# Performance work log

Hardware: AMD Instinct MI355X
Metric: run time of the kernel (lower is better)

Reference implementation:

```python
import jax, jax.numpy as jnp
import numpy as np
import itertools

VOXEL_SIZE = np.array([0.05, 0.05, 0.1], np.float32)   # xyz, from cfg.voxel_size
GRID_OFFSET = np.array([0.0, -40.0, -3.0], np.float32)  # xyz, cfg.grid_bounds[:3]
BN_EPS = 1e-3

# ---------------- rulebook construction (numpy, mirrors spconv indice pairs) ----------------

def _enc(c, shape):
    Z, Y, X = shape
    c = c.astype(np.int64)
    return ((c[:, 0] * Z + c[:, 1]) * Y + c[:, 2]) * X + c[:, 3]

def _lookup(sk, order, q):
    pos = np.clip(np.searchsorted(sk, q), 0, len(sk) - 1)
    return np.where((q >= 0) & (sk[pos] == q), order[pos], -1).astype(np.int32)

def _subm_rulebook(coords, shape):
    # submanifold conv k=3, pad=1: output sites == input sites; neighbor = out + (k-1)
    keys = _enc(coords, shape)
    order = np.argsort(keys).astype(np.int32)
    sk = keys[order]
    dims = np.array(shape)
    rows = []
    for off in itertools.product((-1, 0, 1), repeat=3):
        nb = coords[:, 1:] + np.array(off)
        inb = ((nb >= 0) & (nb < dims)).all(1)
        full = np.concatenate([coords[:, :1], nb], 1)
        q = np.where(inb, _enc(full, shape), -1)
        rows.append(_lookup(sk, order, q))
    return np.stack(rows)  # [27, N] input index or -1

def _strided_rulebook(coords, shape_in, ksize, stride, pad):
    # regular sparse conv: out active = any site receiving a contribution; in = out*s - p + k
    ksize = np.array(ksize); stride = np.array(stride); pad = np.array(pad)
    shape_out = tuple((((np.array(shape_in) + 2 * pad - ksize) // stride) + 1).tolist())
    keys = _enc(coords, shape_in)
    order = np.argsort(keys).astype(np.int32)
    sk = keys[order]
    cand = []
    for k in itertools.product(*[range(int(x)) for x in ksize]):
        num = coords[:, 1:] + pad - np.array(k)
        ok = (num % stride == 0).all(1)
        o = num // stride
        ok &= (o >= 0).all(1) & (o < np.array(shape_out)).all(1)
        cand.append(np.concatenate([coords[ok, :1], o[ok]], 1))
    out_coords = np.unique(np.concatenate(cand, 0), axis=0).astype(np.int32)
    dims_in = np.array(shape_in)
    rows = []
    for k in itertools.product(*[range(int(x)) for x in ksize]):
        ic = out_coords[:, 1:] * stride - pad + np.array(k)
        inb = ((ic >= 0) & (ic < dims_in)).all(1)
        full = np.concatenate([out_coords[:, :1], ic], 1)
        q = np.where(inb, _enc(full, shape_in), -1)
        rows.append(_lookup(sk, order, q))
    return out_coords, np.stack(rows), shape_out

# ---------------- inputs ----------------

def setup_inputs() -> dict:
    rng = np.random.default_rng(0)
    B, NPB = 2, 8000
    shape0 = (41, 1600, 1280)
    parts = []
    for b in range(B):
        c = np.stack([rng.integers(0, shape0[0], 4 * NPB),
                      rng.integers(0, shape0[1], 4 * NPB),
                      rng.integers(0, shape0[2], 4 * NPB)], 1)
        c = np.unique(c, axis=0)[:NPB]
        parts.append(np.concatenate([np.full((len(c), 1), b), c], 1))
    coords0 = np.concatenate(parts, 0).astype(np.int32)

    rb0 = _subm_rulebook(coords0, shape0)
    coords1, rbc1, shape1 = _strided_rulebook(coords0, shape0, (3, 3, 3), (2, 2, 2), (1, 1, 1))
    rb1 = _subm_rulebook(coords1, shape1)
    coords2, rbc2, shape2 = _strided_rulebook(coords1, shape1, (3, 3, 3), (2, 2, 2), (1, 1, 1))
    rb2 = _subm_rulebook(coords2, shape2)
    coords3, rbc3, shape3 = _strided_rulebook(coords2, shape2, (3, 3, 3), (2, 2, 2), (0, 1, 1))
    rb3 = _subm_rulebook(coords3, shape3)
    coords4, rbc4, shape4 = _strided_rulebook(coords3, shape3, (3, 1, 1), (2, 1, 1), (0, 0, 0))

    def w(*s):
        return jnp.asarray((rng.standard_normal(s) * 0.1).astype(np.float32))

    inp = {"features": jnp.asarray(rng.standard_normal((len(coords0), 4)).astype(np.float32))}
    specs = [("1a", 27, 4, 16), ("1b", 27, 16, 16), ("1c", 27, 16, 32),
             ("2a", 27, 32, 32), ("2b", 27, 32, 32), ("2c", 27, 32, 64),
             ("3a", 27, 64, 64), ("3b", 27, 64, 64), ("3c", 27, 64, 64), ("3d", 27, 64, 64),
             ("4a", 27, 64, 64), ("4b", 27, 64, 64), ("4c", 27, 64, 64), ("4d", 3, 64, 64)]
    for name, K, ci, co in specs:
        inp["w" + name] = w(K, ci, co)
        inp["g" + name] = jnp.asarray((np.abs(rng.standard_normal(co)) + 0.5).astype(np.float32))
        inp["b" + name] = jnp.asarray((rng.standard_normal(co) * 0.1).astype(np.float32))
    inp.update(coordinates=jnp.asarray(coords0), coords1=jnp.asarray(coords1),
               coords2=jnp.asarray(coords2), coords3=jnp.asarray(coords3),
               rb0=jnp.asarray(rb0), rbc1=jnp.asarray(rbc1), rb1=jnp.asarray(rb1),
               rbc2=jnp.asarray(rbc2), rb2=jnp.asarray(rb2), rbc3=jnp.asarray(rbc3),
               rb3=jnp.asarray(rb3), rbc4=jnp.asarray(rbc4), batch_size=B)
    return inp

# ---------------- forward math ----------------

def _sconv(feat, rb, W):
    # gather-GEMM-scatter: rb[k,n] = input row feeding output n via kernel offset k (-1 = none)
    out = jnp.zeros((rb.shape[1], W.shape[2]), feat.dtype)
    for k in range(W.shape[0]):
        idx = rb[k]
        g = jnp.where(idx[:, None] >= 0, feat[jnp.clip(idx, 0)], 0.0)
        out = out + g @ W[k]
    return out

def _bn_relu(x, g, b):
    # BatchNorm1d in training mode over active voxels (biased var), eps=1e-3, then ReLU
    m = jnp.mean(x, 0)
    v = jnp.mean(jnp.square(x - m), 0)
    return jax.nn.relu((x - m) * (g / jnp.sqrt(v + BN_EPS)) + b)

def reference(features, w1a, g1a, b1a, w1b, g1b, b1b, w1c, g1c, b1c,
              w2a, g2a, b2a, w2b, g2b, b2b, w2c, g2c, b2c,
              w3a, g3a, b3a, w3b, g3b, b3b, w3c, g3c, b3c, w3d, g3d, b3d,
              w4a, g4a, b4a, w4b, g4b, b4b, w4c, g4c, b4c, w4d, g4d, b4d,
              coordinates, coords1, coords2, coords3,
              rb0, rbc1, rb1, rbc2, rb2, rbc3, rb3, rbc4, batch_size):
    f0 = features
    h = _bn_relu(_sconv(f0, rb0, w1a), g1a, b1a)
    h = _bn_relu(_sconv(h, rb0, w1b), g1b, b1b)
    f1 = _bn_relu(_sconv(h, rbc1, w1c), g1c, b1c)
    h = _bn_relu(_sconv(f1, rb1, w2a), g2a, b2a)
    h = _bn_relu(_sconv(h, rb1, w2b), g2b, b2b)
    f2 = _bn_relu(_sconv(h, rbc2, w2c), g2c, b2c)
    h = _bn_relu(_sconv(f2, rb2, w3a), g3a, b3a)
    h = _bn_relu(_sconv(h, rb2, w3b), g3b, b3b)
    h = _bn_relu(_sconv(h, rb2, w3c), g3c, b3c)
    f3 = _bn_relu(_sconv(h, rbc3, w3d), g3d, b3d)
    h = _bn_relu(_sconv(f3, rb3, w4a), g4a, b4a)
    h = _bn_relu(_sconv(h, rb3, w4b), g4b, b4b)
    h = _bn_relu(_sconv(h, rb3, w4c), g4c, b4c)
    f4 = _bn_relu(_sconv(h, rbc4, w4d), g4d, b4d)

    vs = jnp.asarray(VOXEL_SIZE)
    off = jnp.asarray(GRID_OFFSET)
    def to_global(stride, c):
        # indices are (b,z,y,x); flip -> (x,y,z,b); take xyz
        return jnp.flip(c, 1)[:, :3].astype(jnp.float32) * (vs * stride) + off
    xyz0 = to_global(1, coordinates)
    xyz1 = to_global(2, coords1)
    xyz2 = to_global(4, coords2)
    xyz3 = to_global(8, coords3)
    return (xyz0, f0, xyz1, f1, xyz2, f2, xyz3, f3, f4)
```

## Files before the change

### kernel.cpp

```cpp
#include <hip/hip_runtime.h>

#define BN_EPS 1e-3f
#define NREP 16

typedef __attribute__((ext_vector_type(8))) short short8;
typedef __attribute__((ext_vector_type(4))) float float4v;

__device__ __forceinline__ short f2bf(float f) {
    unsigned u = __float_as_uint(f);
    unsigned r = (u + 0x7FFFu + ((u >> 16) & 1u)) >> 16;
    return (short)r;
}

template <int N>
__device__ __forceinline__ void waitcnt_vm() {
    __builtin_amdgcn_s_waitcnt(0xF70 | (N & 15) | ((N >> 4) << 14));
}

__device__ __forceinline__ void wave_barrier() { asm volatile("s_barrier" ::: "memory"); }

__device__ __forceinline__ void dma16(const short* g, short* l) {
    __builtin_amdgcn_global_load_lds((const __attribute__((address_space(1))) void*)g,
                                     (__attribute__((address_space(3))) void*)l, 16, 0, 0);
}


__global__ __launch_bounds__(256) void zero_kernel(float* p, int n) {
    int i = blockIdx.x * 256 + threadIdx.x;
    if (i < n) p[i] = 0.f;
}

__global__ __launch_bounds__(256) void copy_kernel(const float* __restrict__ in,
                                                   float* __restrict__ out, int n) {
    int i = blockIdx.x * 256 + threadIdx.x;
    if (i < n) out[i] = in[i];
}

__global__ __launch_bounds__(256) void zero_rows_kernel(short* a, short* b, long maxN) {
    int t = threadIdx.x;
    if (t < 32) a[maxN * 32 + t] = 0;
    else if (t < 96) a[maxN * 64 + (t - 32)] = 0;
    else if (t < 128) b[maxN * 32 + (t - 96)] = 0;
    else if (t < 192) b[maxN * 64 + (t - 128)] = 0;
}

__global__ __launch_bounds__(256) void xyz_kernel(const int* __restrict__ coords,
                                                  float* __restrict__ out, int N,
                                                  float sx, float sy, float sz) {
    int n = blockIdx.x * 256 + threadIdx.x;
    if (n >= N) return;
    int4 c = ((const int4*)coords)[n];
    out[n * 3 + 0] = c.w * sx;
    out[n * 3 + 1] = c.z * sy - 40.0f;
    out[n * 3 + 2] = c.y * sz - 3.0f;
}

__global__ __launch_bounds__(256) void convert_f0(const float* __restrict__ f,
                                                  short* __restrict__ dst, int N) {
    int i = blockIdx.x * 256 + threadIdx.x;
    if (i >= N * 32) return;
    int c = i & 31, n = i >> 5;
    dst[i] = (c < 4) ? f2bf(f[n * 4 + c]) : (short)0;
}

struct PrepAll {
    const float* src[14];
    short* dst[14];
    int CI[14];
    int CO[14];
    int CHP[14];
    int cum[15];
};

__global__ __launch_bounds__(256) void prep_all_kernel(PrepAll d) {
    int i = blockIdx.x * 256 + threadIdx.x;
    if (i >= d.cum[14]) return;
    int l = 0;
    while (l < 13 && i >= d.cum[l + 1]) ++l;
    int f = i - d.cum[l];
    int CO = d.CO[l], CI = d.CI[l];
    int NCH = d.CHP[l] / 32, CT = CO / 16;
    int e = f & 7;
    int u = f >> 3;
    int l16 = u & 15;
    int q = (u >> 4) & 3;
    int u2 = u >> 6;
    int t = u2 % CT;
    int c = (u2 / CT) % NCH;
    int k = u2 / (CT * NCH);
    int ci = c * 32 + q * 8 + e;
    int co = t * 16 + l16;
    float v = (ci < CI) ? d.src[l][((size_t)k * CI + ci) * CO + co] : 0.f;
    d.dst[l][f] = f2bf(v);
}

struct ASet {
    short8 v0, v1, v2, v3;
};

template <int CHP, int CO, int K>
__global__ __launch_bounds__(256, 4) void sconv_hyb(const short* __restrict__ feat,
                                                    const int* __restrict__ rb,
                                                    const short* __restrict__ Wt,
                                                    float* __restrict__ out,
                                                    float* __restrict__ stats, int N, int zrow) {
    constexpr int NCH = CHP / 32;
    constexpr int CT = CO / 16;
    constexpr int BTILE = CO * CHP;
    constexpr int NB = BTILE / 512;
    constexpr int A = 2 * NCH;
    constexpr int ROWS = 128;

    __shared__ __align__(16) short ldsB[3 * BTILE];
    __shared__ int sIdx[K * ROWS];
    __shared__ int sFlag[K];
    __shared__ int sKl[K];
    __shared__ int sKn;

    const int tid = threadIdx.x;
    const int w = tid >> 6;
    const int lane = tid & 63;
    const int quad = lane >> 4;
    const int l16 = lane & 15;
    const int m0 = blockIdx.x * ROWS;

    if (tid < K) sFlag[tid] = 0;
    __syncthreads();
    for (int e = tid; e < K * ROWS; e += 256) {
        int r = m0 + (e & (ROWS - 1));
        int v = (r < N) ? rb[(size_t)(e >> 7) * N + r] : -1;
        sIdx[e] = v;
        if (v >= 0) sFlag[e >> 7] = 1;
    }
    __syncthreads();
    if (w == 0) {
        int f = (lane < K) ? sFlag[lane] : 0;
        unsigned long long m = __ballot(f != 0);
        if (f) sKl[__popcll(m & ((1ull << lane) - 1ull))] = lane;
        if (lane == 0) sKn = (int)__popcll(m);
    }
    __syncthreads();
    const int nk = sKn;

    const short* fquad = feat + quad * 8;

    auto issueB = [&](int kp, int slot) {
        const short* wk = Wt + (size_t)kp * BTILE + lane * 8;
        short* bb = ldsB + slot * BTILE;
#pragma unroll
        for (int jj = 0; jj < (NB + 3) / 4; ++jj) {
            int j = jj * 4 + w;
            if (j < NB) dma16(wk + j * 512, bb + j * 512);
        }
    };
    auto issueA = [&](int kp) {
        ASet s;
        int i0 = sIdx[kp * ROWS + w * 32 + l16];
        int i1 = sIdx[kp * ROWS + w * 32 + 16 + l16];
        const short* p0 = fquad + (size_t)(i0 < 0 ? zrow : i0) * CHP;
        const short* p1 = fquad + (size_t)(i1 < 0 ? zrow : i1) * CHP;
        s.v0 = *(const short8*)p0;
        s.v2 = *(const short8*)p1;
        if constexpr (NCH == 2) {
            s.v1 = *(const short8*)(p0 + 32);
            s.v3 = *(const short8*)(p1 + 32);
        } else {
            s.v1 = (short8)0;
            s.v3 = (short8)0;
        }
        return s;
    };

    float4v acc[2][CT];
#pragma unroll
    for (int mt = 0; mt < 2; ++mt)
#pragma unroll
        for (int t = 0; t < CT; ++t) acc[mt][t] = (float4v)0.f;

    constexpr int BW0 = NB / 4 + ((NB % 4) > 0 ? 1 : 0);
    constexpr int BW1 = NB / 4 + ((NB % 4) > 1 ? 1 : 0);
    constexpr int BW2 = NB / 4 + ((NB % 4) > 2 ? 1 : 0);
    constexpr int BW3 = NB / 4;

    ASet sA{}, sB{}, sC{};
    if (nk > 0) {
        issueB(sKl[0], 0);
        sA = issueA(sKl[0]);
    }
    if (nk > 1) {
        issueB(sKl[1], 1);
        sB = issueA(sKl[1]);
    }

    int slotRd = 0, slotWr = 2;
    for (int i = 0; i < nk; ++i) {
        if (i < nk - 1) {
            if (w == 0) waitcnt_vm<BW0 + A>();
            else if (w == 1) waitcnt_vm<BW1 + A>();
            else if (w == 2) waitcnt_vm<BW2 + A>();
            else waitcnt_vm<BW3 + A>();
        } else {
            waitcnt_vm<0>();
        }
        __builtin_amdgcn_sched_barrier(0);
        wave_barrier();
        if (i + 2 < nk) {
            issueB(sKl[i + 2], slotWr);
            sC = issueA(sKl[i + 2]);
        }
        const short* bb = ldsB + slotRd * BTILE;
#pragma unroll
        for (int c = 0; c < NCH; ++c) {
#pragma unroll
            for (int t = 0; t < CT; ++t) {
                short8 bf = *(const short8*)(bb + ((c * CT + t) * 64 + quad * 16 + l16) * 8);
#pragma unroll
                for (int mt = 0; mt < 2; ++mt) {
                    short8 af = (mt == 0) ? ((c == 0) ? sA.v0 : sA.v1)
                                          : ((c == 0) ? sA.v2 : sA.v3);
                    acc[mt][t] = __builtin_amdgcn_mfma_f32_16x16x32_bf16(af, bf, acc[mt][t], 0,
                                                                         0, 0);
                }
            }
        }
        sA = sB;
        sB = sC;
        slotRd = (slotRd == 2) ? 0 : slotRd + 1;
        slotWr = (slotWr == 2) ? 0 : slotWr + 1;
    }

#pragma unroll
    for (int mt = 0; mt < 2; ++mt)
#pragma unroll
        for (int t = 0; t < CT; ++t) {
            int col = t * 16 + l16;
#pragma unroll
            for (int r = 0; r < 4; ++r) {
                int orow = m0 + w * 32 + mt * 16 + quad * 4 + r;
                if (orow < N) out[(size_t)orow * CO + col] = acc[mt][t][r];
            }
        }

    __syncthreads();
    float* red = (float*)ldsB;
#pragma unroll
    for (int t = 0; t < CT; ++t) {
        float s = 0.f, ss = 0.f;
#pragma unroll
        for (int mt = 0; mt < 2; ++mt)
#pragma unroll
            for (int r = 0; r < 4; ++r) {
                float v = acc[mt][t][r];
                s += v;
                ss += v * v;
            }
        s += __shfl_xor(s, 16);
        s += __shfl_xor(s, 32);
        ss += __shfl_xor(ss, 16);
        ss += __shfl_xor(ss, 32);
        if (lane < 16) {
            red[w * 2 * CO + t * 16 + lane] = s;
            red[w * 2 * CO + CO + t * 16 + lane] = ss;
        }
    }
    __syncthreads();
    if (tid < 2 * CO) {
        float v = red[tid] + red[2 * CO + tid] + red[4 * CO + tid] + red[6 * CO + tid];
        float* st = stats + (size_t)(blockIdx.x & (NREP - 1)) * 128;
        atomicAdd(&st[(tid < CO) ? tid : (64 + tid - CO)], v);
    }
}

template <int COUT, int CHPN, bool F32OUT, bool BFOUT>
__global__ __launch_bounds__(256) void bn_apply(const float* __restrict__ x,
                                                const float* __restrict__ stats,
                                                const float* __restrict__ g,
                                                const float* __restrict__ b,
                                                float* __restrict__ fout,
                                                short* __restrict__ bfout, int N) {
    constexpr int CW = BFOUT ? CHPN : COUT;
    __shared__ float ssc[COUT];
    __shared__ float ssh[COUT];
    int tid = threadIdx.x;
    if (tid < COUT) {
        float s = 0.f, q = 0.f;
#pragma unroll
        for (int r = 0; r < NREP; ++r) {
            s += stats[r * 128 + tid];
            q += stats[r * 128 + 64 + tid];
        }
        float inv = 1.0f / (float)N;
        float m = s * inv;
        float v = q * inv - m * m;
        float sc = g[tid] / sqrtf(v + BN_EPS);
        ssc[tid] = sc;
        ssh[tid] = b[tid] - m * sc;
    }
    __syncthreads();
    long i = (long)blockIdx.x * 256 + tid;
    if (i >= (long)N * CW) return;
    int c = (int)(i % CW);
    long n = i / CW;
    float y = 0.f;
    if (c < COUT) {
        y = fmaxf(x[n * COUT + c] * ssc[c] + ssh[c], 0.f);
        if (F32OUT) __builtin_nontemporal_store(y, &fout[n * COUT + c]);
    }
    if (BFOUT) bfout[n * CHPN + c] = f2bf(y);
}


template <int CHP, int CO, int K>
static void conv(const short* fin, const int* rb, const short* wt, float* preact, float* stats,
                 int N, int zrow, hipStream_t stream) {
    dim3 grid((N + 127) / 128);
    hipLaunchKernelGGL((sconv_hyb<CHP, CO, K>), grid, dim3(256), 0, stream, fin, rb, wt, preact,
                       stats, N, zrow);
}

template <int COUT, int CHPN, bool F32OUT, bool BFOUT>
static void apply(const float* preact, const float* stats, const float* g, const float* b,
                  float* fout, short* bfout, int N, hipStream_t stream) {
    constexpr int CW = BFOUT ? CHPN : COUT;
    int blocks = (int)(((long)N * CW + 255) / 256);
    hipLaunchKernelGGL((bn_apply<COUT, CHPN, F32OUT, BFOUT>), dim3(blocks), dim3(256), 0, stream,
                       preact, stats, g, b, fout, bfout, N);
}

extern "C" void kernel_launch(void* const* d_in, const int* in_sizes, int n_in, void* d_out,
                              int out_size, void* d_ws, size_t ws_size, hipStream_t stream) {
    const float* features = (const float*)d_in[0];
    const float* W[14];
    const float* G[14];
    const float* Bb[14];
    for (int i = 0; i < 14; ++i) {
        W[i] = (const float*)d_in[1 + 3 * i];
        G[i] = (const float*)d_in[2 + 3 * i];
        Bb[i] = (const float*)d_in[3 + 3 * i];
    }
    const int* coords0 = (const int*)d_in[43];
    const int* coords1 = (const int*)d_in[44];
    const int* coords2 = (const int*)d_in[45];
    const int* coords3 = (const int*)d_in[46];
    const int* rb0 = (const int*)d_in[47];
    const int* rbc1 = (const int*)d_in[48];
    const int* rb1 = (const int*)d_in[49];
    const int* rbc2 = (const int*)d_in[50];
    const int* rb2 = (const int*)d_in[51];
    const int* rbc3 = (const int*)d_in[52];
    const int* rb3 = (const int*)d_in[53];
    const int* rbc4 = (const int*)d_in[54];

    const int N0 = in_sizes[0] / 4;
    const int N1 = in_sizes[44] / 4;
    const int N2 = in_sizes[45] / 4;
    const int N3 = in_sizes[46] / 4;
    const int N4 = in_sizes[54] / 3;

    float* out = (float*)d_out;
    long off = 0;
    float* xyz0 = out + off; off += (long)N0 * 3;
    float* f0   = out + off; off += (long)N0 * 4;
    float* xyz1 = out + off; off += (long)N1 * 3;
    float* f1   = out + off; off += (long)N1 * 32;
    float* xyz2 = out + off; off += (long)N2 * 3;
    float* f2   = out + off; off += (long)N2 * 64;
    float* xyz3 = out + off; off += (long)N3 * 3;
    float* f3   = out + off; off += (long)N3 * 64;
    float* f4   = out + off;

    long maxN = N0;
    if (N1 > maxN) maxN = N1;
    if (N2 > maxN) maxN = N2;
    if (N3 > maxN) maxN = N3;
    if (N4 > maxN) maxN = N4;
    const int zrow = (int)maxN;

    float* preact = (float*)d_ws;
    float* statsBase = preact + (size_t)maxN * 64;
    short* bfA = (short*)(statsBase + 14 * NREP * 128);
    short* bfB = bfA + (size_t)(maxN + 1) * 64;
    short* wtBase = bfB + (size_t)(maxN + 1) * 64;

    static const int KK[14] = {27, 27, 27, 27, 27, 27, 27, 27, 27, 27, 27, 27, 27, 3};
    static const int CI[14] = {4, 16, 16, 32, 32, 32, 64, 64, 64, 64, 64, 64, 64, 64};
    static const int CO[14] = {16, 16, 32, 32, 32, 64, 64, 64, 64, 64, 64, 64, 64, 64};
    short* WT[14];
    PrepAll pd;
    {
        size_t o = 0;
        int cum = 0;
        for (int l = 0; l < 14; ++l) {
            WT[l] = wtBase + o;
            int chp = CI[l] <= 32 ? 32 : 64;
            pd.src[l] = W[l];
            pd.dst[l] = WT[l];
            pd.CI[l] = CI[l];
            pd.CO[l] = CO[l];
            pd.CHP[l] = chp;
            pd.cum[l] = cum;
            cum += KK[l] * CO[l] * chp;
            o += (size_t)KK[l] * CO[l] * chp;
        }
        pd.cum[14] = cum;
    }

    int nstats = 14 * NREP * 128;
    hipLaunchKernelGGL(zero_kernel, dim3((nstats + 255) / 256), dim3(256), 0, stream, statsBase,
                       nstats);
    hipLaunchKernelGGL(zero_rows_kernel, dim3(1), dim3(256), 0, stream, bfA, bfB, maxN);
    hipLaunchKernelGGL(prep_all_kernel, dim3((pd.cum[14] + 255) / 256), dim3(256), 0, stream, pd);

    hipLaunchKernelGGL(copy_kernel, dim3((N0 * 4 + 255) / 256), dim3(256), 0, stream, features, f0,
                       N0 * 4);
    hipLaunchKernelGGL(xyz_kernel, dim3((N0 + 255) / 256), dim3(256), 0, stream, coords0, xyz0, N0,
                       0.05f, 0.05f, 0.1f);
    hipLaunchKernelGGL(xyz_kernel, dim3((N1 + 255) / 256), dim3(256), 0, stream, coords1, xyz1, N1,
                       0.1f, 0.1f, 0.2f);
    hipLaunchKernelGGL(xyz_kernel, dim3((N2 + 255) / 256), dim3(256), 0, stream, coords2, xyz2, N2,
                       0.2f, 0.2f, 0.4f);
    hipLaunchKernelGGL(xyz_kernel, dim3((N3 + 255) / 256), dim3(256), 0, stream, coords3, xyz3, N3,
                       0.4f, 0.4f, 0.8f);
    hipLaunchKernelGGL(convert_f0, dim3((N0 * 32 + 255) / 256), dim3(256), 0, stream, features,
                       bfA, N0);

    float* st = statsBase;
#define STAT(l) (st + (size_t)(l)*NREP * 128)

    conv<32, 16, 27>(bfA, rb0, WT[0], preact, STAT(0), N0, zrow, stream);
    apply<16, 32, false, true>(preact, STAT(0), G[0], Bb[0], nullptr, bfB, N0, stream);
    conv<32, 16, 27>(bfB, rb0, WT[1], preact, STAT(1), N0, zrow, stream);
    apply<16, 32, false, true>(preact, STAT(1), G[1], Bb[1], nullptr, bfA, N0, stream);
    conv<32, 32, 27>(bfA, rbc1, WT[2], preact, STAT(2), N1, zrow, stream);
    apply<32, 32, true, true>(preact, STAT(2), G[2], Bb[2], f1, bfB, N1, stream);

    conv<32, 32, 27>(bfB, rb1, WT[3], preact, STAT(3), N1, zrow, stream);
    apply<32, 32, false, true>(preact, STAT(3), G[3], Bb[3], nullptr, bfA, N1, stream);
    conv<32, 32, 27>(bfA, rb1, WT[4], preact, STAT(4), N1, zrow, stream);
    apply<32, 32, false, true>(preact, STAT(4), G[4], Bb[4], nullptr, bfB, N1, stream);
    conv<32, 64, 27>(bfB, rbc2, WT[5], preact, STAT(5), N2, zrow, stream);
    apply<64, 64, true, true>(preact, STAT(5), G[5], Bb[5], f2, bfA, N2, stream);

    conv<64, 64, 27>(bfA, rb2, WT[6], preact, STAT(6), N2, zrow, stream);
    apply<64, 64, false, true>(preact, STAT(6), G[6], Bb[6], nullptr, bfB, N2, stream);
    conv<64, 64, 27>(bfB, rb2, WT[7], preact, STAT(7), N2, zrow, stream);
    apply<64, 64, false, true>(preact, STAT(7), G[7], Bb[7], nullptr, bfA, N2, stream);
    conv<64, 64, 27>(bfA, rb2, WT[8], preact, STAT(8), N2, zrow, stream);
    apply<64, 64, false, true>(preact, STAT(8), G[8], Bb[8], nullptr, bfB, N2, stream);
    conv<64, 64, 27>(bfB, rbc3, WT[9], preact, STAT(9), N3, zrow, stream);
    apply<64, 64, true, true>(preact, STAT(9), G[9], Bb[9], f3, bfA, N3, stream);

    conv<64, 64, 27>(bfA, rb3, WT[10], preact, STAT(10), N3, zrow, stream);
    apply<64, 64, false, true>(preact, STAT(10), G[10], Bb[10], nullptr, bfB, N3, stream);
    conv<64, 64, 27>(bfB, rb3, WT[11], preact, STAT(11), N3, zrow, stream);
    apply<64, 64, false, true>(preact, STAT(11), G[11], Bb[11], nullptr, bfA, N3, stream);
    conv<64, 64, 27>(bfA, rb3, WT[12], preact, STAT(12), N3, zrow, stream);
    apply<64, 64, false, true>(preact, STAT(12), G[12], Bb[12], nullptr, bfB, N3, stream);
    conv<64, 64, 3>(bfB, rbc4, WT[13], preact, STAT(13), N4, zrow, stream);
    apply<64, 64, true, false>(preact, STAT(13), G[13], Bb[13], f4, nullptr, N4, stream);
#undef STAT
}
```

Measured before the change: 733.1 us.

## Double conv block to 8 waves/256 rows and vectorize BN apply by 8

The sparse conv kernel now uses 512 threads over 256 output rows per block. This spreads each weight tile load across 8 waves and amortizes it over twice as many rows, and the per-wave wait counts are recomputed to match. The BN apply kernel now handles 8 channels per thread with vector float4 loads and stores and packed bf16 stores, cutting thread count and memory transactions. Rulebook loads also become nontemporal. Risks include lower occupancy with larger blocks, higher LDS use for sIdx, and more idle rows in sparse tail blocks.

```diff
diff --git a/kernel.cpp b/kernel.cpp
--- a/kernel.cpp
+++ b/kernel.cpp
@@ -99,7 +99,7 @@
 };
 
 template <int CHP, int CO, int K>
-__global__ __launch_bounds__(256, 4) void sconv_hyb(const short* __restrict__ feat,
+__global__ __launch_bounds__(512, 4) void sconv_hyb(const short* __restrict__ feat,
                                                     const int* __restrict__ rb,
                                                     const short* __restrict__ Wt,
                                                     float* __restrict__ out,
@@ -109,7 +109,10 @@
     constexpr int BTILE = CO * CHP;
     constexpr int NB = BTILE / 512;
     constexpr int A = 2 * NCH;
-    constexpr int ROWS = 128;
+    constexpr int ROWS = 256;
+    constexpr int WAVES = 8;
+    constexpr int B0 = NB / WAVES;
+    constexpr int BR = NB % WAVES;
 
     __shared__ __align__(16) short ldsB[3 * BTILE];
     __shared__ int sIdx[K * ROWS];
@@ -126,11 +129,11 @@
 
     if (tid < K) sFlag[tid] = 0;
     __syncthreads();
-    for (int e = tid; e < K * ROWS; e += 256) {
+    for (int e = tid; e < K * ROWS; e += 512) {
         int r = m0 + (e & (ROWS - 1));
-        int v = (r < N) ? rb[(size_t)(e >> 7) * N + r] : -1;
+        int v = (r < N) ? __builtin_nontemporal_load(&rb[(size_t)(e >> 8) * N + r]) : -1;
         sIdx[e] = v;
-        if (v >= 0) sFlag[e >> 7] = 1;
+        if (v >= 0) sFlag[e >> 8] = 1;
     }
     __syncthreads();
     if (w == 0) {
@@ -148,8 +151,8 @@
         const short* wk = Wt + (size_t)kp * BTILE + lane * 8;
         short* bb = ldsB + slot * BTILE;
 #pragma unroll
-        for (int jj = 0; jj < (NB + 3) / 4; ++jj) {
-            int j = jj * 4 + w;
+        for (int jj = 0; jj < (NB + WAVES - 1) / WAVES; ++jj) {
+            int j = jj * WAVES + w;
             if (j < NB) dma16(wk + j * 512, bb + j * 512);
         }
     };
@@ -177,11 +180,6 @@
 #pragma unroll
         for (int t = 0; t < CT; ++t) acc[mt][t] = (float4v)0.f;
 
-    constexpr int BW0 = NB / 4 + ((NB % 4) > 0 ? 1 : 0);
-    constexpr int BW1 = NB / 4 + ((NB % 4) > 1 ? 1 : 0);
-    constexpr int BW2 = NB / 4 + ((NB % 4) > 2 ? 1 : 0);
-    constexpr int BW3 = NB / 4;
-
     ASet sA{}, sB{}, sC{};
     if (nk > 0) {
         issueB(sKl[0], 0);
@@ -195,10 +193,8 @@
     int slotRd = 0, slotWr = 2;
     for (int i = 0; i < nk; ++i) {
         if (i < nk - 1) {
-            if (w == 0) waitcnt_vm<BW0 + A>();
-            else if (w == 1) waitcnt_vm<BW1 + A>();
-            else if (w == 2) waitcnt_vm<BW2 + A>();
-            else waitcnt_vm<BW3 + A>();
+            if (BR > 0 && w < BR) waitcnt_vm<B0 + 1 + A>();
+            else waitcnt_vm<B0 + A>();
         } else {
             waitcnt_vm<0>();
         }
@@ -265,7 +261,9 @@
     }
     __syncthreads();
     if (tid < 2 * CO) {
-        float v = red[tid] + red[2 * CO + tid] + red[4 * CO + tid] + red[6 * CO + tid];
+        float v = 0.f;
+#pragma unroll
+        for (int r = 0; r < WAVES; ++r) v += red[r * 2 * CO + tid];
         float* st = stats + (size_t)(blockIdx.x & (NREP - 1)) * 128;
         atomicAdd(&st[(tid < CO) ? tid : (64 + tid - CO)], v);
     }
@@ -279,6 +277,7 @@
                                                 float* __restrict__ fout,
                                                 short* __restrict__ bfout, int N) {
     constexpr int CW = BFOUT ? CHPN : COUT;
+    constexpr int CV = CW / 8;
     __shared__ float ssc[COUT];
     __shared__ float ssh[COUT];
     int tid = threadIdx.x;
@@ -298,23 +297,53 @@
     }
     __syncthreads();
     long i = (long)blockIdx.x * 256 + tid;
-    if (i >= (long)N * CW) return;
-    int c = (int)(i % CW);
-    long n = i / CW;
-    float y = 0.f;
-    if (c < COUT) {
-        y = fmaxf(x[n * COUT + c] * ssc[c] + ssh[c], 0.f);
-        if (F32OUT) __builtin_nontemporal_store(y, &fout[n * COUT + c]);
-    }
-    if (BFOUT) bfout[n * CHPN + c] = f2bf(y);
+    if (i >= (long)N * CV) return;
+    int c8 = (int)(i % CV);
+    long n = i / CV;
+    int cb = c8 * 8;
+    float y[8];
+#pragma unroll
+    for (int j = 0; j < 8; ++j) y[j] = 0.f;
+    if (cb < COUT) {
+        const float4v* xr = (const float4v*)(x + n * COUT + cb);
+        float4v a0 = xr[0];
+        float4v a1 = xr[1];
+#pragma unroll
+        for (int j = 0; j < 4; ++j) {
+            y[j] = fmaxf(a0[j] * ssc[cb + j] + ssh[cb + j], 0.f);
+            y[4 + j] = fmaxf(a1[j] * ssc[cb + 4 + j] + ssh[cb + 4 + j], 0.f);
+        }
+        if constexpr (F32OUT) {
+            float* fo = fout + n * COUT + cb;
+            if ((((unsigned long long)fout) & 15ull) == 0) {
+                float4v o0, o1;
+#pragma unroll
+                for (int j = 0; j < 4; ++j) {
+                    o0[j] = y[j];
+                    o1[j] = y[4 + j];
+                }
+                ((float4v*)fo)[0] = o0;
+                ((float4v*)fo)[1] = o1;
+            } else {
+#pragma unroll
+                for (int j = 0; j < 8; ++j) fo[j] = y[j];
+            }
+        }
+    }
+    if constexpr (BFOUT) {
+        short8 p;
+#pragma unroll
+        for (int j = 0; j < 8; ++j) p[j] = f2bf(y[j]);
+        *(short8*)(bfout + n * CHPN + cb) = p;
+    }
 }
 
 
 template <int CHP, int CO, int K>
 static void conv(const short* fin, const int* rb, const short* wt, float* preact, float* stats,
                  int N, int zrow, hipStream_t stream) {
-    dim3 grid((N + 127) / 128);
-    hipLaunchKernelGGL((sconv_hyb<CHP, CO, K>), grid, dim3(256), 0, stream, fin, rb, wt, preact,
+    dim3 grid((N + 255) / 256);
+    hipLaunchKernelGGL((sconv_hyb<CHP, CO, K>), grid, dim3(512), 0, stream, fin, rb, wt, preact,
                        stats, N, zrow);
 }
 
@@ -322,7 +351,8 @@
 static void apply(const float* preact, const float* stats, const float* g, const float* b,
                   float* fout, short* bfout, int N, hipStream_t stream) {
     constexpr int CW = BFOUT ? CHPN : COUT;
-    int blocks = (int)(((long)N * CW + 255) / 256);
+    constexpr int CV = CW / 8;
+    int blocks = (int)(((long)N * CV + 255) / 256);
     hipLaunchKernelGGL((bn_apply<COUT, CHPN, F32OUT, BFOUT>), dim3(blocks), dim3(256), 0, stream,
                        preact, stats, g, b, fout, bfout, N);
 }
```

Result: no change. 721.0 us (-1.7%).
